# Performance work log

Hardware: AMD Instinct MI355X
Metric: run time of the kernel (lower is better)

The kernel has to match this reference:

```python
import math
import jax, jax.numpy as jnp
import numpy as np

B, N, D, E, DN, H, M = 32, 64, 256, 32, 64, 8, 32
EPS = 1e-5


def _ln(x):
    # param-free layer norm over the last axis
    mu = jnp.mean(x, axis=-1, keepdims=True)
    var = jnp.var(x, axis=-1, keepdims=True)
    return (x - mu) * jax.lax.rsqrt(var + EPS)


def setup_inputs() -> dict:
    key = jax.random.key(0)
    ks = jax.random.split(key, 9)
    embeddings = jax.random.normal(ks[0], (B, N, D), dtype=jnp.float32)
    edge_features = jax.random.normal(ks[1], (B, N, N, E), dtype=jnp.float32)
    mask = jax.random.randint(ks[2], (B, N), 0, 2).astype(bool)
    node_features = jax.random.normal(ks[3], (B, N, DN), dtype=jnp.float32)
    s = lambda d: 1.0 / math.sqrt(d)
    W_edge = jax.random.normal(ks[4], (E, H, M), dtype=jnp.float32) * s(E)
    W_recv = jax.random.normal(ks[5], (D, H, M), dtype=jnp.float32) * s(D)
    W_send = jax.random.normal(ks[6], (D, H, M), dtype=jnp.float32) * s(D)
    W_recv_node = jax.random.normal(ks[7], (DN, H, M), dtype=jnp.float32) * s(DN)
    W_send_node = jax.random.normal(ks[8], (DN, H, M), dtype=jnp.float32) * s(DN)
    return dict(embeddings=embeddings, edge_features=edge_features, mask=mask,
                node_features=node_features, W_edge=W_edge, W_recv=W_recv,
                W_send=W_send, W_recv_node=W_recv_node, W_send_node=W_send_node)


def reference(embeddings, edge_features, mask, node_features,
              W_edge, W_recv, W_send, W_recv_node, W_send_node):
    sqrt2 = math.sqrt(2.0)
    mask_f = mask.astype(embeddings.dtype)  # [B, N]
    emb = _ln(embeddings) * mask_f[..., None]  # [B, N, D]
    # double mask: [B, sender, receiver, 1]
    dm = (mask_f[..., None, :, None] * mask_f[..., :, None, None])
    ef = edge_features * dm  # [B, N, N, E]
    # projections to (heads, message_dim)
    edge_part = jnp.einsum('bije,ehm->bijhm', ef, W_edge)        # [B,N,N,H,M]
    recv = jnp.einsum('bjd,dhm->bjhm', emb, W_recv) / sqrt2      # [B,N,H,M]
    send = jnp.einsum('bid,dhm->bihm', emb, W_send) / sqrt2
    # receiver broadcast over sender axis (-4), sender over receiver axis (-3)
    rs = jnp.tanh(recv[..., None, :, :, :] + send[..., :, None, :, :])  # [B,N,N,H,M]
    rn = jnp.einsum('bjd,dhm->bjhm', node_features, W_recv_node)
    sn = jnp.einsum('bid,dhm->bihm', node_features, W_send_node)
    rs = rs * jax.nn.sigmoid((rn[..., None, :, :, :] + sn[..., :, None, :, :]) / sqrt2)
    msgs = rs * edge_part * dm[..., None]  # [B,N,N,H,M]
    updates = msgs.sum(axis=-4)            # sum over senders -> [B,N,H,M]
    updates = _ln(updates)
    return jnp.reshape(updates, (*updates.shape[:-2], -1))  # [B,N,H*M]
```

## Files before the change

kernel.cpp:

```cpp
#include <hip/hip_runtime.h>
#include <hip/hip_bf16.h>
#include <math.h>

#define B_   32
#define N_   64
#define D_   256
#define E_   32
#define DN_  64
#define H_   8
#define M_   32
#define HM_  256
#define BN_  2048
#define EPS_ 1e-5f
#define SQRT2_    1.41421356237309515f
#define NINVSQ2_ (-0.70710678118654752f)

typedef float f32x4 __attribute__((ext_vector_type(4)));
typedef short bf16x8 __attribute__((ext_vector_type(8)));
union U4S8 { uint4 u; bf16x8 s; };

__device__ __forceinline__ unsigned pk2(float a, float b) {
    union { __hip_bfloat162 h; unsigned u; } cv;
    cv.h = __float22bfloat162_rn(make_float2(a, b));
    return cv.u;
}


__device__ __forceinline__ void remap512(int wg, int& b, int& s) {
    b = (wg & 7) * 4 + (wg >> 7);
    s = (wg >> 3) & 15;
}
__device__ __forceinline__ void remap1024(int wg, int& b, int& s) {
    b = (wg & 7) * 4 + (wg >> 8);
    s = (wg >> 3) & 31;
}

__device__ __forceinline__ unsigned long long mask_bits(
        const int* mraw, int b, int t, int w, int l, int* s_flag_sh,
        unsigned long long* bits_sh) {
    if (t == 0) *s_flag_sh = 0;
    __syncthreads();
    { const int ti = t & 255;
      int v0 = mraw[ti], v1 = mraw[ti + 256];
      if (((v0 | v1) & ~1) != 0) atomicOr(s_flag_sh, 1); }
    __syncthreads();
    const bool bytef = (*s_flag_sh != 0);
    const unsigned char* mbb = (const unsigned char*)mraw;
    if (w == 0) {
        const int k = b * N_ + l;
        const bool on = bytef ? (mbb[k] != 0) : (mraw[k] != 0);
        unsigned long long bits = __ballot(on);
        if (l == 0) *bits_sh = bits;
    }
    __syncthreads();
    return *bits_sh;
}

__global__ __launch_bounds__(512, 4) void node_k(
        const float* __restrict__ emb, const float* __restrict__ nfeat,
        const int* __restrict__ mraw,
        const float* __restrict__ Wr, const float* __restrict__ Ws,
        const float* __restrict__ Wrn, const float* __restrict__ Wsn,
        float2* __restrict__ g_rr, float2* __restrict__ g_ssC) {
    const int t = threadIdx.x;
    const int w = t >> 6, l = t & 63, hi = l >> 4, lo = l & 15;
    const int rt = w & 3;
    const int sendside = w >> 2;
    int b, s; remap512(blockIdx.x, b, s);

    __shared__ int s_flag;
    __shared__ unsigned long long bits_sh;
    const unsigned long long bits = mask_bits(mraw, b, t, w, l, &s_flag, &bits_sh);
    const int cb = __popcll(bits);

    float mu_l, rs_l;
    {
        const int qrow = rt * 16 + (l >> 2);
        const float* rp = emb + (size_t)(b * N_ + qrow) * D_ + (l & 3) * 64;
        float sv = 0.f, s2 = 0.f;
        #pragma unroll
        for (int k = 0; k < 16; ++k) {
            float4 x = *(const float4*)(rp + k * 4);
            sv += x.x + x.y + x.z + x.w;
            s2 += x.x*x.x + x.y*x.y + x.z*x.z + x.w*x.w;
        }
        sv += __shfl_xor(sv, 1); sv += __shfl_xor(sv, 2);
        s2 += __shfl_xor(s2, 1); s2 += __shfl_xor(s2, 2);
        float mu  = sv * (1.0f / D_);
        float var = s2 * (1.0f / D_) - mu * mu;
        float rs  = rsqrtf(var + EPS_) * (((bits >> qrow) & 1ull) ? 1.0f : 0.0f);
        mu_l = __shfl(mu, lo << 2);
        rs_l = __shfl(rs, lo << 2);
    }

    const float* W1 = sendside ? Ws  : Wr;
    const float* W2 = sendside ? Wsn : Wrn;
    const int nb = s * 16 + lo;
    const float* arow = emb   + (size_t)(b * N_ + rt * 16 + lo) * D_  + hi * 8;
    const float* nrow = nfeat + (size_t)(b * N_ + rt * 16 + lo) * DN_ + hi * 8;
    f32x4 a1 = {0,0,0,0}, a2 = {0,0,0,0};
    #pragma unroll
    for (int ks = 0; ks < 8; ++ks) {
        float4 xa = *(const float4*)(arow + ks * 32);
        float4 xb = *(const float4*)(arow + ks * 32 + 4);
        U4S8 a;
        a.u = make_uint4(pk2((xa.x - mu_l) * rs_l, (xa.y - mu_l) * rs_l),
                         pk2((xa.z - mu_l) * rs_l, (xa.w - mu_l) * rs_l),
                         pk2((xb.x - mu_l) * rs_l, (xb.y - mu_l) * rs_l),
                         pk2((xb.z - mu_l) * rs_l, (xb.w - mu_l) * rs_l));
        const float* wp = W1 + (size_t)(ks * 32 + hi * 8) * HM_ + nb;
        U4S8 bfr;
        bfr.u = make_uint4(pk2(wp[0],     wp[HM_]),    pk2(wp[2*HM_], wp[3*HM_]),
                           pk2(wp[4*HM_], wp[5*HM_]),  pk2(wp[6*HM_], wp[7*HM_]));
        a1 = __builtin_amdgcn_mfma_f32_16x16x32_bf16(a.s, bfr.s, a1, 0, 0, 0);
        if (ks < 2) {
            float4 na  = *(const float4*)(nrow + ks * 32);
            float4 nb4 = *(const float4*)(nrow + ks * 32 + 4);
            U4S8 an;
            an.u = make_uint4(pk2(na.x, na.y),   pk2(na.z, na.w),
                              pk2(nb4.x, nb4.y), pk2(nb4.z, nb4.w));
            const float* wn = W2 + (size_t)(ks * 32 + hi * 8) * HM_ + nb;
            U4S8 bn;
            bn.u = make_uint4(pk2(wn[0],     wn[HM_]),    pk2(wn[2*HM_], wn[3*HM_]),
                              pk2(wn[4*HM_], wn[5*HM_]),  pk2(wn[6*HM_], wn[7*HM_]));
            a2 = __builtin_amdgcn_mfma_f32_16x16x32_bf16(an.s, bn.s, a2, 0, 0, 0);
        }
    }

    #pragma unroll
    for (int r = 0; r < 4; ++r) {
        const int i = rt * 16 + hi * 4 + r;
        float2 v = make_float2(__expf(SQRT2_ * a1[r]), __expf(NINVSQ2_ * a2[r]));
        if (sendside == 0) {
            g_rr[(size_t)(b * N_ + i) * HM_ + nb] = v;
        } else if ((bits >> i) & 1ull) {
            const int p = __popcll(bits & ((1ull << i) - 1ull));
            g_ssC[(size_t)(b * N_ + p) * HM_ + nb] = v;
        }
    }
    if (sendside) {
        const int tt = t - 256;
        for (int p = cb + (tt >> 4); p < N_; p += 16)
            g_ssC[(size_t)(b * N_ + p) * HM_ + s * 16 + (tt & 15)] = make_float2(0.f, 0.f);
    }
}

__global__ __launch_bounds__(256, 4) void edge_k(
        const float* __restrict__ edge, const float* __restrict__ We,
        const int* __restrict__ mraw,
        const float2* __restrict__ g_rr, const float2* __restrict__ g_ssC,
        float* __restrict__ out) {
    const int t = threadIdx.x;
    const int w = t >> 6, l = t & 63, hi = l >> 4, lo = l & 15;
    int b, s; remap1024(blockIdx.x, b, s);
    const int j0 = s * 2;

    __shared__ int s_flag;
    __shared__ unsigned long long bits_sh;
    __shared__ int sidx_s[N_];
    __shared__ __align__(16) uint4 ldsA[2][256];

    const unsigned long long bits = mask_bits(mraw, b, t, w, l, &s_flag, &bits_sh);
    const int cb = __popcll(bits);
    if (w == 0) {
        const bool on = (bits >> l) & 1ull;
        int p = __popcll(bits & ((1ull << l) - 1ull));
        if (on) sidx_s[p] = l;
        if (l >= cb) sidx_s[l] = -1;
    }
    __syncthreads();

    if (((bits >> j0) & 3ull) == 0ull) {
        #pragma unroll
        for (int q = 0; q < 2; ++q)
            out[(size_t)(b * N_ + j0 + q) * HM_ + t] = 0.0f;
        return;
    }

    {
        const int mt = t >> 6, phi = (t >> 4) & 3, plo = t & 15;
        const int si = sidx_s[mt * 16 + plo];
        if (si >= 0) {
            const float* rb = edge + ((size_t)((b * N_ + si) * N_ + j0)) * E_ + phi * 8;
            #pragma unroll
            for (int q = 0; q < 2; ++q) {
                float4 v0 = *(const float4*)(rb + q * E_);
                float4 v1 = *(const float4*)(rb + q * E_ + 4);
                ldsA[q][t] = make_uint4(pk2(v0.x, v0.y), pk2(v0.z, v0.w),
                                        pk2(v1.x, v1.y), pk2(v1.z, v1.w));
            }
        } else {
            #pragma unroll
            for (int q = 0; q < 2; ++q) ldsA[q][t] = make_uint4(0, 0, 0, 0);
        }
    }
    __syncthreads();

    U4S8 b4[4];
    #pragma unroll
    for (int nl = 0; nl < 4; ++nl) {
        const float* wp = We + (size_t)(hi * 8) * HM_ + w * 64 + nl * 16 + lo;
        b4[nl].u = make_uint4(pk2(wp[0],     wp[HM_]),    pk2(wp[2*HM_], wp[3*HM_]),
                              pk2(wp[4*HM_], wp[5*HM_]),  pk2(wp[6*HM_], wp[7*HM_]));
    }

    float2 rrq[2][4];
    #pragma unroll
    for (int q = 0; q < 2; ++q)
        #pragma unroll
        for (int nl = 0; nl < 4; ++nl)
            rrq[q][nl] = g_rr[(size_t)(b * N_ + j0 + q) * HM_ + w * 64 + nl * 16 + lo];

    float upd[2][4];
    #pragma unroll
    for (int q = 0; q < 2; ++q)
        #pragma unroll
        for (int nl = 0; nl < 4; ++nl) upd[q][nl] = 0.0f;

    const f32x4 zero = {0.0f, 0.0f, 0.0f, 0.0f};
    #pragma unroll
    for (int mt = 0; mt < 4; ++mt) {
        if (mt * 16 < cb) {
            f32x4 acc[2][4];
            #pragma unroll
            for (int q = 0; q < 2; ++q) {
                U4S8 a; a.u = ldsA[q][mt * 64 + l];
                #pragma unroll
                for (int nl = 0; nl < 4; ++nl)
                    acc[q][nl] = __builtin_amdgcn_mfma_f32_16x16x32_bf16(a.s, b4[nl].s, zero, 0, 0, 0);
            }
            #pragma unroll
            for (int r = 0; r < 4; ++r) {
                const float2* srow =
                    g_ssC + (size_t)(b * N_ + mt * 16 + hi * 4 + r) * HM_ + w * 64 + lo;
                float2 ssv[4];
                #pragma unroll
                for (int nl = 0; nl < 4; ++nl) ssv[nl] = srow[nl * 16];
                #pragma unroll
                for (int q = 0; q < 2; ++q)
                    #pragma unroll
                    for (int nl = 0; nl < 4; ++nl) {
                        float u = rrq[q][nl].x * ssv[nl].x;
                        float v = rrq[q][nl].y * ssv[nl].y;
                        float den = (u + 1.0f) * (v + 1.0f);
                        float g = (u - 1.0f) * __builtin_amdgcn_rcpf(den);
                        upd[q][nl] = fmaf(g, acc[q][nl][r], upd[q][nl]);
                    }
            }
        }
    }
    #pragma unroll
    for (int q = 0; q < 2; ++q) {
        const int j = j0 + q, bn = b * N_ + j;
        if (!((bits >> j) & 1ull)) {
            out[(size_t)bn * HM_ + w * 64 + l] = 0.0f;
            continue;
        }
        float u0 = upd[q][0], u1 = upd[q][1], u2 = upd[q][2], u3 = upd[q][3];
        u0 += __shfl_xor(u0, 16); u0 += __shfl_xor(u0, 32);
        u1 += __shfl_xor(u1, 16); u1 += __shfl_xor(u1, 32);
        u2 += __shfl_xor(u2, 16); u2 += __shfl_xor(u2, 32);
        u3 += __shfl_xor(u3, 16); u3 += __shfl_xor(u3, 32);
        float s0 = u0 + u1, q0 = u0*u0 + u1*u1;
        float s1 = u2 + u3, q1 = u2*u2 + u3*u3;
        #pragma unroll
        for (int k = 8; k >= 1; k >>= 1) {
            s0 += __shfl_xor(s0, k); q0 += __shfl_xor(q0, k);
            s1 += __shfl_xor(s1, k); q1 += __shfl_xor(q1, k);
        }
        float mu0 = s0 * (1.0f / M_), va0 = q0 * (1.0f / M_) - mu0 * mu0;
        float mu1 = s1 * (1.0f / M_), va1 = q1 * (1.0f / M_) - mu1 * mu1;
        float rs0 = rsqrtf(va0 + EPS_), rs1 = rsqrtf(va1 + EPS_);
        float v01 = (hi & 1) ? u1 : u0;
        float v23 = (hi & 1) ? u3 : u2;
        float val = (hi < 2) ? v01 : v23;
        float o = (hi < 2) ? (val - mu0) * rs0 : (val - mu1) * rs1;
        out[(size_t)bn * HM_ + w * 64 + l] = o;
    }
}

extern "C" void kernel_launch(void* const* d_in, const int* in_sizes, int n_in,
                              void* d_out, int out_size, void* d_ws, size_t ws_size,
                              hipStream_t stream) {
    const float* embeddings = (const float*)d_in[0];
    const float* edge_feat  = (const float*)d_in[1];
    const int*   mask_raw   = (const int*)d_in[2];
    const float* node_feat  = (const float*)d_in[3];
    const float* W_edge     = (const float*)d_in[4];
    const float* W_recv     = (const float*)d_in[5];
    const float* W_send     = (const float*)d_in[6];
    const float* W_recvn    = (const float*)d_in[7];
    const float* W_sendn    = (const float*)d_in[8];
    float* out = (float*)d_out;

    float2* g_ssC = (float2*)d_ws;
    float2* g_rr  = g_ssC + (size_t)BN_ * HM_;

    node_k<<<512, 512, 0, stream>>>(embeddings, node_feat, mask_raw,
                                    W_recv, W_send, W_recvn, W_sendn,
                                    g_rr, g_ssC);
    edge_k<<<1024, 256, 0, stream>>>(edge_feat, W_edge, mask_raw,
                                     g_rr, g_ssC, out);
}
```

Before: 39.06 us.

## Process four receivers per block with 8 waves each owning one head

```diff
diff --git a/kernel.cpp b/kernel.cpp
--- a/kernel.cpp
+++ b/kernel.cpp
@@ -29,10 +29,6 @@
 __device__ __forceinline__ void remap512(int wg, int& b, int& s) {
     b = (wg & 7) * 4 + (wg >> 7);
     s = (wg >> 3) & 15;
-}
-__device__ __forceinline__ void remap1024(int wg, int& b, int& s) {
-    b = (wg & 7) * 4 + (wg >> 8);
-    s = (wg >> 3) & 31;
 }
 
 __device__ __forceinline__ unsigned long long mask_bits(
@@ -145,20 +141,20 @@
     }
 }
 
-__global__ __launch_bounds__(256, 4) void edge_k(
+__global__ __launch_bounds__(512, 2) void edge_k(
         const float* __restrict__ edge, const float* __restrict__ We,
         const int* __restrict__ mraw,
         const float2* __restrict__ g_rr, const float2* __restrict__ g_ssC,
         float* __restrict__ out) {
     const int t = threadIdx.x;
     const int w = t >> 6, l = t & 63, hi = l >> 4, lo = l & 15;
-    int b, s; remap1024(blockIdx.x, b, s);
-    const int j0 = s * 2;
+    int b, s; remap512(blockIdx.x, b, s);
+    const int j0 = s * 4;
 
     __shared__ int s_flag;
     __shared__ unsigned long long bits_sh;
     __shared__ int sidx_s[N_];
-    __shared__ __align__(16) uint4 ldsA[2][256];
+    __shared__ __align__(16) uint4 ldsA[4][256];
 
     const unsigned long long bits = mask_bits(mraw, b, t, w, l, &s_flag, &bits_sh);
     const int cb = __popcll(bits);
@@ -170,112 +166,113 @@
     }
     __syncthreads();
 
-    if (((bits >> j0) & 3ull) == 0ull) {
-        #pragma unroll
-        for (int q = 0; q < 2; ++q)
-            out[(size_t)(b * N_ + j0 + q) * HM_ + t] = 0.0f;
+    if (((bits >> j0) & 15ull) == 0ull) {
+        if (hi < 2) {
+            #pragma unroll
+            for (int q = 0; q < 4; ++q)
+                out[(size_t)(b * N_ + j0 + q) * HM_ + w * 32 + hi * 16 + lo] = 0.0f;
+        }
         return;
     }
 
     {
-        const int mt = t >> 6, phi = (t >> 4) & 3, plo = t & 15;
+        const int tt = t & 255;
+        const int mt = tt >> 6, phi = (tt >> 4) & 3, plo = tt & 15;
+        const int qp = t >> 8;
         const int si = sidx_s[mt * 16 + plo];
         if (si >= 0) {
-            const float* rb = edge + ((size_t)((b * N_ + si) * N_ + j0)) * E_ + phi * 8;
+            const float* rb = edge + ((size_t)((b * N_ + si) * N_ + j0 + qp * 2)) * E_ + phi * 8;
             #pragma unroll
-            for (int q = 0; q < 2; ++q) {
-                float4 v0 = *(const float4*)(rb + q * E_);
-                float4 v1 = *(const float4*)(rb + q * E_ + 4);
-                ldsA[q][t] = make_uint4(pk2(v0.x, v0.y), pk2(v0.z, v0.w),
-                                        pk2(v1.x, v1.y), pk2(v1.z, v1.w));
+            for (int qq = 0; qq < 2; ++qq) {
+                float4 v0 = *(const float4*)(rb + qq * E_);
+                float4 v1 = *(const float4*)(rb + qq * E_ + 4);
+                ldsA[qp * 2 + qq][tt] = make_uint4(pk2(v0.x, v0.y), pk2(v0.z, v0.w),
+                                                   pk2(v1.x, v1.y), pk2(v1.z, v1.w));
             }
         } else {
-            #pragma unroll
-            for (int q = 0; q < 2; ++q) ldsA[q][t] = make_uint4(0, 0, 0, 0);
-        }
-    }
-    __syncthreads();
-
-    U4S8 b4[4];
-    #pragma unroll
-    for (int nl = 0; nl < 4; ++nl) {
-        const float* wp = We + (size_t)(hi * 8) * HM_ + w * 64 + nl * 16 + lo;
+            ldsA[qp * 2 + 0][tt] = make_uint4(0, 0, 0, 0);
+            ldsA[qp * 2 + 1][tt] = make_uint4(0, 0, 0, 0);
+        }
+    }
+    __syncthreads();
+
+    U4S8 b4[2];
+    #pragma unroll
+    for (int nl = 0; nl < 2; ++nl) {
+        const float* wp = We + (size_t)(hi * 8) * HM_ + w * 32 + nl * 16 + lo;
         b4[nl].u = make_uint4(pk2(wp[0],     wp[HM_]),    pk2(wp[2*HM_], wp[3*HM_]),
                               pk2(wp[4*HM_], wp[5*HM_]),  pk2(wp[6*HM_], wp[7*HM_]));
     }
 
-    float2 rrq[2][4];
-    #pragma unroll
-    for (int q = 0; q < 2; ++q)
+    float2 rrq[4][2];
+    #pragma unroll
+    for (int q = 0; q < 4; ++q)
         #pragma unroll
-        for (int nl = 0; nl < 4; ++nl)
-            rrq[q][nl] = g_rr[(size_t)(b * N_ + j0 + q) * HM_ + w * 64 + nl * 16 + lo];
-
-    float upd[2][4];
-    #pragma unroll
-    for (int q = 0; q < 2; ++q)
-        #pragma unroll
-        for (int nl = 0; nl < 4; ++nl) upd[q][nl] = 0.0f;
+        for (int nl = 0; nl < 2; ++nl)
+            rrq[q][nl] = g_rr[(size_t)(b * N_ + j0 + q) * HM_ + w * 32 + nl * 16 + lo];
+
+    float upd[4][2];
+    #pragma unroll
+    for (int q = 0; q < 4; ++q) { upd[q][0] = 0.0f; upd[q][1] = 0.0f; }
 
     const f32x4 zero = {0.0f, 0.0f, 0.0f, 0.0f};
     #pragma unroll
     for (int mt = 0; mt < 4; ++mt) {
         if (mt * 16 < cb) {
-            f32x4 acc[2][4];
+            f32x4 acc[4][2];
             #pragma unroll
-            for (int q = 0; q < 2; ++q) {
+            for (int q = 0; q < 4; ++q) {
                 U4S8 a; a.u = ldsA[q][mt * 64 + l];
                 #pragma unroll
-                for (int nl = 0; nl < 4; ++nl)
+                for (int nl = 0; nl < 2; ++nl)
                     acc[q][nl] = __builtin_amdgcn_mfma_f32_16x16x32_bf16(a.s, b4[nl].s, zero, 0, 0, 0);
             }
             #pragma unroll
             for (int r = 0; r < 4; ++r) {
                 const float2* srow =
-                    g_ssC + (size_t)(b * N_ + mt * 16 + hi * 4 + r) * HM_ + w * 64 + lo;
-                float2 ssv[4];
+                    g_ssC + (size_t)(b * N_ + mt * 16 + hi * 4 + r) * HM_ + w * 32 + lo;
+                float2 ssv0 = srow[0], ssv1 = srow[16];
                 #pragma unroll
-                for (int nl = 0; nl < 4; ++nl) ssv[nl] = srow[nl * 16];
-                #pragma unroll
-                for (int q = 0; q < 2; ++q)
-                    #pragma unroll
-                    for (int nl = 0; nl < 4; ++nl) {
-                        float u = rrq[q][nl].x * ssv[nl].x;
-                        float v = rrq[q][nl].y * ssv[nl].y;
-                        float den = (u + 1.0f) * (v + 1.0f);
-                        float g = (u - 1.0f) * __builtin_amdgcn_rcpf(den);
-                        upd[q][nl] = fmaf(g, acc[q][nl][r], upd[q][nl]);
+                for (int q = 0; q < 4; ++q) {
+                    {
+                        float u = rrq[q][0].x * ssv0.x;
+                        float v = rrq[q][0].y * ssv0.y;
+                        float g = (u - 1.0f) * __builtin_amdgcn_rcpf((u + 1.0f) * (v + 1.0f));
+                        upd[q][0] = fmaf(g, acc[q][0][r], upd[q][0]);
                     }
+                    {
+                        float u = rrq[q][1].x * ssv1.x;
+                        float v = rrq[q][1].y * ssv1.y;
+                        float g = (u - 1.0f) * __builtin_amdgcn_rcpf((u + 1.0f) * (v + 1.0f));
+                        upd[q][1] = fmaf(g, acc[q][1][r], upd[q][1]);
+                    }
+                }
             }
         }
     }
-    #pragma unroll
-    for (int q = 0; q < 2; ++q) {
+
+    #pragma unroll
+    for (int q = 0; q < 4; ++q) {
         const int j = j0 + q, bn = b * N_ + j;
         if (!((bits >> j) & 1ull)) {
-            out[(size_t)bn * HM_ + w * 64 + l] = 0.0f;
+            if (hi < 2)
+                out[(size_t)bn * HM_ + w * 32 + hi * 16 + lo] = 0.0f;
             continue;
         }
-        float u0 = upd[q][0], u1 = upd[q][1], u2 = upd[q][2], u3 = upd[q][3];
+        float u0 = upd[q][0], u1 = upd[q][1];
         u0 += __shfl_xor(u0, 16); u0 += __shfl_xor(u0, 32);
         u1 += __shfl_xor(u1, 16); u1 += __shfl_xor(u1, 32);
-        u2 += __shfl_xor(u2, 16); u2 += __shfl_xor(u2, 32);
-        u3 += __shfl_xor(u3, 16); u3 += __shfl_xor(u3, 32);
-        float s0 = u0 + u1, q0 = u0*u0 + u1*u1;
-        float s1 = u2 + u3, q1 = u2*u2 + u3*u3;
+        float sv = u0 + u1, qs = u0 * u0 + u1 * u1;
         #pragma unroll
         for (int k = 8; k >= 1; k >>= 1) {
-            s0 += __shfl_xor(s0, k); q0 += __shfl_xor(q0, k);
-            s1 += __shfl_xor(s1, k); q1 += __shfl_xor(q1, k);
-        }
-        float mu0 = s0 * (1.0f / M_), va0 = q0 * (1.0f / M_) - mu0 * mu0;
-        float mu1 = s1 * (1.0f / M_), va1 = q1 * (1.0f / M_) - mu1 * mu1;
-        float rs0 = rsqrtf(va0 + EPS_), rs1 = rsqrtf(va1 + EPS_);
-        float v01 = (hi & 1) ? u1 : u0;
-        float v23 = (hi & 1) ? u3 : u2;
-        float val = (hi < 2) ? v01 : v23;
-        float o = (hi < 2) ? (val - mu0) * rs0 : (val - mu1) * rs1;
-        out[(size_t)bn * HM_ + w * 64 + l] = o;
+            sv += __shfl_xor(sv, k); qs += __shfl_xor(qs, k);
+        }
+        float mu = sv * (1.0f / M_), va = qs * (1.0f / M_) - mu * mu;
+        float rs = rsqrtf(va + EPS_);
+        if (hi < 2) {
+            float val = hi ? u1 : u0;
+            out[(size_t)bn * HM_ + w * 32 + hi * 16 + lo] = (val - mu) * rs;
+        }
     }
 }
 
@@ -299,6 +296,6 @@
     node_k<<<512, 512, 0, stream>>>(embeddings, node_feat, mask_raw,
                                     W_recv, W_send, W_recvn, W_sendn,
                                     g_rr, g_ssC);
-    edge_k<<<1024, 256, 0, stream>>>(edge_feat, W_edge, mask_raw,
-                                     g_rr, g_ssC, out);
-}
+    edge_k<<<512, 512, 0, stream>>>(edge_feat, W_edge, mask_raw,
+                                    g_rr, g_ssC, out);
+}
```

Result: no change. 39.45 us (+1.0%).
